# Performance work log

Measured on AMD Instinct MI355X. Metric: run time of the kernel, lower is better.

Reference implementation:

```python
import jax, jax.numpy as jnp
import numpy as np

B, N, D = 4, 4096, 1024

def setup_inputs() -> dict:
    key = jax.random.key(0)
    kx, kql, kqr, kk, kv = jax.random.split(key, 5)
    std = 1.0 / D
    return {
        "x": jax.random.normal(kx, (B, N, D), dtype=jnp.float32),
        "w_query_left": jax.random.normal(kql, (D, D), dtype=jnp.float32) * std,
        "w_query_right": jax.random.normal(kqr, (D, D), dtype=jnp.float32) * std,
        "w_key": jax.random.normal(kk, (D, D), dtype=jnp.float32) * std,
        "w_value": jax.random.normal(kv, (D, D), dtype=jnp.float32) * std,
    }

def reference(x, w_query_left, w_query_right, w_key, w_value):
    # Four dxd projections
    query_left = jnp.einsum('bnd,de->bne', x, w_query_left)
    query_right = jnp.einsum('bnd,de->bne', x, w_query_right)
    key = jnp.einsum('bnd,de->bne', x, w_key)
    value = jnp.einsum('bnd,de->bne', x, w_value)
    # Elementwise gate
    query = query_left * query_right
    # Kernelized attention: key^T @ value, then query @ kv  (dropout p=0 in eval)
    kv_attn = jnp.einsum('bnd,bne->bde', key, value)   # [B, D, D]
    linear_attn = jnp.einsum('bnd,bde->bne', query, kv_attn)
    return linear_attn
```

## Files before the change

kernel.cpp:

```cpp
#include <hip/hip_runtime.h>
#include <stdint.h>

typedef short bf16x8 __attribute__((ext_vector_type(8)));
typedef float f32x4 __attribute__((ext_vector_type(4)));

__device__ __forceinline__ uint16_t f2b(float f) {
    uint32_t u = __builtin_bit_cast(uint32_t, f);
    return (uint16_t)((u + 0x7fffu + ((u >> 16) & 1u)) >> 16);
}

__device__ __forceinline__ void gll16(const void* g, void* l) {
    __builtin_amdgcn_global_load_lds(
        (const __attribute__((address_space(1))) uint32_t*)(uintptr_t)g,
        (__attribute__((address_space(3))) uint32_t*)(uint32_t)(uintptr_t)l,
        16, 0, 0);
}

__global__ __launch_bounds__(256) void cvt_f32_bf16(const float4* __restrict__ in,
                                                    uint2* __restrict__ out, int nvec) {
    int i = blockIdx.x * 256 + threadIdx.x;
    if (i >= nvec) return;
    float4 v = in[i];
    uint2 o;
    o.x = (uint32_t)f2b(v.x) | ((uint32_t)f2b(v.y) << 16);
    o.y = (uint32_t)f2b(v.z) | ((uint32_t)f2b(v.w) << 16);
    out[i] = o;
}

struct Ptr4 { const float* p[4]; };

__global__ __launch_bounds__(256) void tr_w(Ptr4 wp, uint16_t* __restrict__ out) {
    const int m = blockIdx.z;
    const float* in = wp.p[m];
    uint16_t* o = out + (size_t)m * 1048576;
    __shared__ uint16_t tile[64][68];
    int t = threadIdx.x;
    int r0 = blockIdx.y * 64, c0 = blockIdx.x * 64;
    for (int p = 0; p < 4; p++) {
        int row = p * 16 + (t >> 4);
        int c4 = (t & 15) * 4;
        float4 v = *(const float4*)&in[(size_t)(r0 + row) * 1024 + c0 + c4];
        tile[row][c4 + 0] = f2b(v.x);
        tile[row][c4 + 1] = f2b(v.y);
        tile[row][c4 + 2] = f2b(v.z);
        tile[row][c4 + 3] = f2b(v.w);
    }
    __syncthreads();
    for (int p = 0; p < 4; p++) {
        int a = p * 16 + (t >> 4);
        int b4 = (t & 15) * 4;
        uint32_t x0 = tile[b4 + 0][a], x1 = tile[b4 + 1][a];
        uint32_t x2 = tile[b4 + 2][a], x3 = tile[b4 + 3][a];
        uint2 pk;
        pk.x = x0 | (x1 << 16);
        pk.y = x2 | (x3 << 16);
        *(uint2*)&o[(size_t)(c0 + a) * 1024 + r0 + b4] = pk;
    }
}

union SmemP {
    struct { uint16_t lA[4096]; uint16_t lB1[4096]; uint16_t lB2[4096]; } s;
    uint16_t tr[8][32][68];
};

__global__ __launch_bounds__(512, 4) void proj512(const uint16_t* __restrict__ A,
                                                  const uint16_t* __restrict__ Wt,
                                                  uint16_t* __restrict__ Q,
                                                  uint16_t* __restrict__ KT,
                                                  uint16_t* __restrict__ VT) {
    __shared__ SmemP u;
    const int t = threadIdx.x;
    const int wave = t >> 6;
    const int lane = t & 63;
    const int m0 = blockIdx.y * 128;
    const int bx = blockIdx.x;
    const int gate = bx < 8;
    const int e0 = (gate ? bx : bx - 8) * 128;
    const uint16_t* B1 = Wt + (size_t)(gate ? 0 : 2) * 1048576 + (size_t)e0 * 1024;
    const uint16_t* B2 = Wt + (size_t)(gate ? 1 : 3) * 1048576 + (size_t)e0 * 1024;
    const int wm = (wave >> 2) * 64;
    const int we = (wave & 3) * 32;

    const uint16_t* gA = A + (size_t)(m0 + (t >> 2)) * 1024 + (t & 3) * 8;
    const uint16_t* gB1 = B1 + (size_t)(t >> 2) * 1024 + (t & 3) * 8;
    const uint16_t* gB2 = B2 + (size_t)(t >> 2) * 1024 + (t & 3) * 8;
    uint16_t* dA = u.s.lA + wave * 512;
    uint16_t* dB1 = u.s.lB1 + wave * 512;
    uint16_t* dB2 = u.s.lB2 + wave * 512;

    f32x4 acc1[4][2] = {};
    f32x4 acc2[4][2] = {};

    const int arow = wm + (lane & 15);
    const int brow = we + (lane & 15);
    const int koff = (lane >> 4) * 8;

    for (int k0 = 0; k0 < 1024; k0 += 32) {
        __syncthreads();
        gll16(gA + k0, dA);
        gll16(gB1 + k0, dB1);
        gll16(gB2 + k0, dB2);
        __syncthreads();

        bf16x8 af[4], b1f[2], b2f[2];
#pragma unroll
        for (int i = 0; i < 4; i++)
            af[i] = *(const bf16x8*)&u.s.lA[(arow + i * 16) * 32 + koff];
#pragma unroll
        for (int j = 0; j < 2; j++)
            b1f[j] = *(const bf16x8*)&u.s.lB1[(brow + j * 16) * 32 + koff];
#pragma unroll
        for (int j = 0; j < 2; j++)
            b2f[j] = *(const bf16x8*)&u.s.lB2[(brow + j * 16) * 32 + koff];
#pragma unroll
        for (int i = 0; i < 4; i++)
#pragma unroll
            for (int j = 0; j < 2; j++) {
                acc1[i][j] = __builtin_amdgcn_mfma_f32_16x16x32_bf16(af[i], b1f[j],
                                                                     acc1[i][j], 0, 0, 0);
                acc2[i][j] = __builtin_amdgcn_mfma_f32_16x16x32_bf16(af[i], b2f[j],
                                                                     acc2[i][j], 0, 0, 0);
            }
    }

    const int rl = (lane >> 4) * 4;
    const int cl = lane & 15;

    if (gate) {
#pragma unroll
        for (int i = 0; i < 4; i++)
#pragma unroll
            for (int j = 0; j < 2; j++)
#pragma unroll
                for (int r = 0; r < 4; r++) {
                    float g = acc1[i][j][r] * acc2[i][j][r];
                    Q[(size_t)(m0 + wm + i * 16 + rl + r) * 1024 + e0 + we + j * 16 + cl] = f2b(g);
                }
    } else {
        __syncthreads();
        const int batch = m0 >> 12;
        const int tok0 = (m0 & 4095) + wm;
        const int fbase = e0 + we;
        uint16_t* outs[2] = {KT, VT};
        for (int s = 0; s < 2; s++) {
            f32x4(*acc)[2] = (s == 0) ? acc1 : acc2;
#pragma unroll
            for (int i = 0; i < 4; i++)
#pragma unroll
                for (int j = 0; j < 2; j++) {
                    int col = j * 16 + cl;
                    int row0 = i * 16 + rl;
                    uint2 pk;
                    pk.x = (uint32_t)f2b(acc[i][j][0]) | ((uint32_t)f2b(acc[i][j][1]) << 16);
                    pk.y = (uint32_t)f2b(acc[i][j][2]) | ((uint32_t)f2b(acc[i][j][3]) << 16);
                    *(uint2*)&u.tr[wave][col][row0] = pk;
                }
            __builtin_amdgcn_s_waitcnt(0);
            uint16_t* O = outs[s] + (size_t)batch * 4194304;
#pragma unroll
            for (int dd = 0; dd < 8; dd++) {
                int f = dd * 4 + (lane >> 4);
                int t4 = cl * 4;
                uint2 v = *(const uint2*)&u.tr[wave][f][t4];
                *(uint2*)&O[(size_t)(fbase + f) * 4096 + tok0 + t4] = v;
            }
            __builtin_amdgcn_s_waitcnt(0);
        }
    }
}

__global__ __launch_bounds__(256) void gemm_kv_splitk(const uint16_t* __restrict__ VT,
                                                      const uint16_t* __restrict__ KT,
                                                      float* __restrict__ P) {
    const int z = blockIdx.z;
    const int batch = z >> 1, ks = z & 1;
    const uint16_t* Ab = VT + (size_t)batch * 4194304 + ks * 2048;
    const uint16_t* Bb = KT + (size_t)batch * 4194304 + ks * 2048;

    __shared__ uint16_t lA[4096];
    __shared__ uint16_t lB[4096];

    const int t = threadIdx.x;
    const int wave = t >> 6;
    const int lane = t & 63;
    const int m0 = blockIdx.y * 128;
    const int n0 = blockIdx.x * 128;
    const int wm = (wave >> 1) * 64;
    const int wn = (wave & 1) * 64;

    const uint16_t* gA0 = Ab + (size_t)(m0 + (t >> 2)) * 4096 + (t & 3) * 8;
    const uint16_t* gB0 = Bb + (size_t)(n0 + (t >> 2)) * 4096 + (t & 3) * 8;
    uint16_t* lA0 = lA + wave * 512;
    uint16_t* lA1 = lA + 2048 + wave * 512;
    uint16_t* lB0 = lB + wave * 512;
    uint16_t* lB1 = lB + 2048 + wave * 512;

    f32x4 acc[4][4] = {};

    const int arow = wm + (lane & 15);
    const int brow = wn + (lane & 15);
    const int koff = (lane >> 4) * 8;

    for (int k0 = 0; k0 < 2048; k0 += 32) {
        __syncthreads();
        gll16(gA0 + k0, lA0);
        gll16(gA0 + (size_t)64 * 4096 + k0, lA1);
        gll16(gB0 + k0, lB0);
        gll16(gB0 + (size_t)64 * 4096 + k0, lB1);
        __syncthreads();

        bf16x8 af[4], bfr[4];
#pragma unroll
        for (int i = 0; i < 4; i++)
            af[i] = *(const bf16x8*)&lA[(arow + i * 16) * 32 + koff];
#pragma unroll
        for (int i = 0; i < 4; i++)
            bfr[i] = *(const bf16x8*)&lB[(brow + i * 16) * 32 + koff];
#pragma unroll
        for (int i = 0; i < 4; i++)
#pragma unroll
            for (int j = 0; j < 4; j++)
                acc[i][j] = __builtin_amdgcn_mfma_f32_16x16x32_bf16(af[i], bfr[j],
                                                                    acc[i][j], 0, 0, 0);
    }

    float* Pb = P + (size_t)z * 1048576;
    const int crow = m0 + wm + (lane >> 4) * 4;
    const int ccol = n0 + wn + (lane & 15);
#pragma unroll
    for (int i = 0; i < 4; i++)
#pragma unroll
        for (int j = 0; j < 4; j++)
#pragma unroll
            for (int r = 0; r < 4; r++)
                Pb[(size_t)(crow + i * 16 + r) * 1024 + ccol + j * 16] = acc[i][j][r];
}

__global__ __launch_bounds__(256) void reduce_kv(const float4* __restrict__ P,
                                                 uint2* __restrict__ kvT) {
    int i = blockIdx.x * 256 + threadIdx.x;
    int b = i >> 18;
    int r = i & 262143;
    const float4* base = P + (size_t)b * 524288 + r;
    float4 s0 = base[0];
    float4 s1 = base[262144];
    float x = s0.x + s1.x;
    float y = s0.y + s1.y;
    float zz = s0.z + s1.z;
    float w = s0.w + s1.w;
    uint2 o;
    o.x = (uint32_t)f2b(x) | ((uint32_t)f2b(y) << 16);
    o.y = (uint32_t)f2b(zz) | ((uint32_t)f2b(w) << 16);
    kvT[i] = o;
}

__global__ __launch_bounds__(256) void gemm_out(const uint16_t* __restrict__ A,
                                                const uint16_t* __restrict__ Bt,
                                                float* __restrict__ C) {
    const uint16_t* Ab = A + (size_t)blockIdx.z * 4194304;
    const uint16_t* Bb = Bt + (size_t)blockIdx.z * 1048576;

    __shared__ uint16_t lA[4096];
    __shared__ uint16_t lB[4096];

    const int t = threadIdx.x;
    const int wave = t >> 6;
    const int lane = t & 63;
    const int m0 = blockIdx.y * 128;
    const int n0 = blockIdx.x * 128;
    const int wm = (wave >> 1) * 64;
    const int wn = (wave & 1) * 64;

    const uint16_t* gA0 = Ab + (size_t)(m0 + (t >> 2)) * 1024 + (t & 3) * 8;
    const uint16_t* gB0 = Bb + (size_t)(n0 + (t >> 2)) * 1024 + (t & 3) * 8;
    uint16_t* lA0 = lA + wave * 512;
    uint16_t* lA1 = lA + 2048 + wave * 512;
    uint16_t* lB0 = lB + wave * 512;
    uint16_t* lB1 = lB + 2048 + wave * 512;

    f32x4 acc[4][4] = {};

    const int arow = wm + (lane & 15);
    const int brow = wn + (lane & 15);
    const int koff = (lane >> 4) * 8;

    for (int k0 = 0; k0 < 1024; k0 += 32) {
        __syncthreads();
        gll16(gA0 + k0, lA0);
        gll16(gA0 + (size_t)64 * 1024 + k0, lA1);
        gll16(gB0 + k0, lB0);
        gll16(gB0 + (size_t)64 * 1024 + k0, lB1);
        __syncthreads();

        bf16x8 af[4], bfr[4];
#pragma unroll
        for (int i = 0; i < 4; i++)
            af[i] = *(const bf16x8*)&lA[(arow + i * 16) * 32 + koff];
#pragma unroll
        for (int i = 0; i < 4; i++)
            bfr[i] = *(const bf16x8*)&lB[(brow + i * 16) * 32 + koff];
#pragma unroll
        for (int i = 0; i < 4; i++)
#pragma unroll
            for (int j = 0; j < 4; j++)
                acc[i][j] = __builtin_amdgcn_mfma_f32_16x16x32_bf16(af[i], bfr[j],
                                                                    acc[i][j], 0, 0, 0);
    }

    float* Cb = C + (size_t)blockIdx.z * 4194304;
    const int crow = m0 + wm + (lane >> 4) * 4;
    const int ccol = n0 + wn + (lane & 15);
#pragma unroll
    for (int i = 0; i < 4; i++)
#pragma unroll
        for (int j = 0; j < 4; j++)
#pragma unroll
            for (int r = 0; r < 4; r++)
                Cb[(size_t)(crow + i * 16 + r) * 1024 + ccol + j * 16] = acc[i][j][r];
}

extern "C" void kernel_launch(void* const* d_in, const int* in_sizes, int n_in,
                              void* d_out, int out_size, void* d_ws, size_t ws_size,
                              hipStream_t stream) {
    const float* x = (const float*)d_in[0];

    uint16_t* ws = (uint16_t*)d_ws;
    uint16_t* xb  = ws;
    float*    kvP = (float*)d_ws;
    uint16_t* Wt  = ws + 33554432;
    uint16_t* kvT = Wt;
    uint16_t* Q   = ws + 37748736;
    uint16_t* KT  = ws + 54525952;
    uint16_t* VT  = ws + 71303168;

    cvt_f32_bf16<<<16384, 256, 0, stream>>>((const float4*)x, (uint2*)xb, 4194304);

    Ptr4 wp;
    wp.p[0] = (const float*)d_in[1];
    wp.p[1] = (const float*)d_in[2];
    wp.p[2] = (const float*)d_in[3];
    wp.p[3] = (const float*)d_in[4];
    tr_w<<<dim3(16, 16, 4), 256, 0, stream>>>(wp, Wt);

    proj512<<<dim3(16, 128), 512, 0, stream>>>(xb, Wt, Q, KT, VT);

    gemm_kv_splitk<<<dim3(8, 8, 8), 256, 0, stream>>>(VT, KT, kvP);

    reduce_kv<<<4096, 256, 0, stream>>>((const float4*)kvP, (uint2*)kvT);

    gemm_out<<<dim3(8, 32, 4), 256, 0, stream>>>(Q, kvT, (float*)d_out);
}
```

Before: 391.2 us.

## Use 512-thread blocks for kv and output GEMMs, raise kv split-K to four

Both the kv GEMM and the output GEMM now run 8 waves per 128x128 tile, each wave computing a 64x32 sub-tile, so a block issues one global-to-LDS load per operand per thread instead of two. The kv GEMM split-K goes from 2 to 4, doubling its block count to 1024 to fill more compute units, and reduce_kv now sums four partials. The cost is more fp32 partial traffic (16 MB written and read instead of 8 MB) and less register-level reuse per wave, since each wave issues 8 MFMAs per 6 LDS fragment loads instead of 16 per 8.

```diff
diff --git a/kernel.cpp b/kernel.cpp
--- a/kernel.cpp
+++ b/kernel.cpp
@@ -169,13 +169,13 @@
     }
 }
 
-__global__ __launch_bounds__(256) void gemm_kv_splitk(const uint16_t* __restrict__ VT,
-                                                      const uint16_t* __restrict__ KT,
-                                                      float* __restrict__ P) {
+__global__ __launch_bounds__(512, 4) void gemm_kv512(const uint16_t* __restrict__ VT,
+                                                     const uint16_t* __restrict__ KT,
+                                                     float* __restrict__ P) {
     const int z = blockIdx.z;
-    const int batch = z >> 1, ks = z & 1;
-    const uint16_t* Ab = VT + (size_t)batch * 4194304 + ks * 2048;
-    const uint16_t* Bb = KT + (size_t)batch * 4194304 + ks * 2048;
+    const int batch = z >> 2, ks = z & 3;
+    const uint16_t* Ab = VT + (size_t)batch * 4194304 + ks * 1024;
+    const uint16_t* Bb = KT + (size_t)batch * 4194304 + ks * 1024;
 
     __shared__ uint16_t lA[4096];
     __shared__ uint16_t lB[4096];
@@ -185,55 +185,51 @@
     const int lane = t & 63;
     const int m0 = blockIdx.y * 128;
     const int n0 = blockIdx.x * 128;
-    const int wm = (wave >> 1) * 64;
-    const int wn = (wave & 1) * 64;
-
-    const uint16_t* gA0 = Ab + (size_t)(m0 + (t >> 2)) * 4096 + (t & 3) * 8;
-    const uint16_t* gB0 = Bb + (size_t)(n0 + (t >> 2)) * 4096 + (t & 3) * 8;
-    uint16_t* lA0 = lA + wave * 512;
-    uint16_t* lA1 = lA + 2048 + wave * 512;
-    uint16_t* lB0 = lB + wave * 512;
-    uint16_t* lB1 = lB + 2048 + wave * 512;
-
-    f32x4 acc[4][4] = {};
+    const int wm = (wave >> 2) * 64;
+    const int we = (wave & 3) * 32;
+
+    const uint16_t* gA = Ab + (size_t)(m0 + (t >> 2)) * 4096 + (t & 3) * 8;
+    const uint16_t* gB = Bb + (size_t)(n0 + (t >> 2)) * 4096 + (t & 3) * 8;
+    uint16_t* dA = lA + wave * 512;
+    uint16_t* dB = lB + wave * 512;
+
+    f32x4 acc[4][2] = {};
 
     const int arow = wm + (lane & 15);
-    const int brow = wn + (lane & 15);
+    const int brow = we + (lane & 15);
     const int koff = (lane >> 4) * 8;
 
-    for (int k0 = 0; k0 < 2048; k0 += 32) {
-        __syncthreads();
-        gll16(gA0 + k0, lA0);
-        gll16(gA0 + (size_t)64 * 4096 + k0, lA1);
-        gll16(gB0 + k0, lB0);
-        gll16(gB0 + (size_t)64 * 4096 + k0, lB1);
-        __syncthreads();
-
-        bf16x8 af[4], bfr[4];
+    for (int k0 = 0; k0 < 1024; k0 += 32) {
+        __syncthreads();
+        gll16(gA + k0, dA);
+        gll16(gB + k0, dB);
+        __syncthreads();
+
+        bf16x8 af[4], bfr[2];
 #pragma unroll
         for (int i = 0; i < 4; i++)
             af[i] = *(const bf16x8*)&lA[(arow + i * 16) * 32 + koff];
 #pragma unroll
-        for (int i = 0; i < 4; i++)
-            bfr[i] = *(const bf16x8*)&lB[(brow + i * 16) * 32 + koff];
-#pragma unroll
-        for (int i = 0; i < 4; i++)
-#pragma unroll
-            for (int j = 0; j < 4; j++)
+        for (int j = 0; j < 2; j++)
+            bfr[j] = *(const bf16x8*)&lB[(brow + j * 16) * 32 + koff];
+#pragma unroll
+        for (int i = 0; i < 4; i++)
+#pragma unroll
+            for (int j = 0; j < 2; j++)
                 acc[i][j] = __builtin_amdgcn_mfma_f32_16x16x32_bf16(af[i], bfr[j],
                                                                     acc[i][j], 0, 0, 0);
     }
 
     float* Pb = P + (size_t)z * 1048576;
-    const int crow = m0 + wm + (lane >> 4) * 4;
-    const int ccol = n0 + wn + (lane & 15);
+    const int rl = (lane >> 4) * 4;
+    const int cl = lane & 15;
 #pragma unroll
     for (int i = 0; i < 4; i++)
 #pragma unroll
-        for (int j = 0; j < 4; j++)
+        for (int j = 0; j < 2; j++)
 #pragma unroll
             for (int r = 0; r < 4; r++)
-                Pb[(size_t)(crow + i * 16 + r) * 1024 + ccol + j * 16] = acc[i][j][r];
+                Pb[(size_t)(m0 + wm + i * 16 + rl + r) * 1024 + n0 + we + j * 16 + cl] = acc[i][j][r];
 }
 
 __global__ __launch_bounds__(256) void reduce_kv(const float4* __restrict__ P,
@@ -241,22 +237,24 @@
     int i = blockIdx.x * 256 + threadIdx.x;
     int b = i >> 18;
     int r = i & 262143;
-    const float4* base = P + (size_t)b * 524288 + r;
+    const float4* base = P + (size_t)b * 1048576 + r;
     float4 s0 = base[0];
     float4 s1 = base[262144];
-    float x = s0.x + s1.x;
-    float y = s0.y + s1.y;
-    float zz = s0.z + s1.z;
-    float w = s0.w + s1.w;
+    float4 s2 = base[524288];
+    float4 s3 = base[786432];
+    float x = s0.x + s1.x + s2.x + s3.x;
+    float y = s0.y + s1.y + s2.y + s3.y;
+    float zz = s0.z + s1.z + s2.z + s3.z;
+    float w = s0.w + s1.w + s2.w + s3.w;
     uint2 o;
     o.x = (uint32_t)f2b(x) | ((uint32_t)f2b(y) << 16);
     o.y = (uint32_t)f2b(zz) | ((uint32_t)f2b(w) << 16);
     kvT[i] = o;
 }
 
-__global__ __launch_bounds__(256) void gemm_out(const uint16_t* __restrict__ A,
-                                                const uint16_t* __restrict__ Bt,
-                                                float* __restrict__ C) {
+__global__ __launch_bounds__(512, 4) void gemm_out512(const uint16_t* __restrict__ A,
+                                                      const uint16_t* __restrict__ Bt,
+                                                      float* __restrict__ C) {
     const uint16_t* Ab = A + (size_t)blockIdx.z * 4194304;
     const uint16_t* Bb = Bt + (size_t)blockIdx.z * 1048576;
 
@@ -268,55 +266,51 @@
     const int lane = t & 63;
     const int m0 = blockIdx.y * 128;
     const int n0 = blockIdx.x * 128;
-    const int wm = (wave >> 1) * 64;
-    const int wn = (wave & 1) * 64;
-
-    const uint16_t* gA0 = Ab + (size_t)(m0 + (t >> 2)) * 1024 + (t & 3) * 8;
-    const uint16_t* gB0 = Bb + (size_t)(n0 + (t >> 2)) * 1024 + (t & 3) * 8;
-    uint16_t* lA0 = lA + wave * 512;
-    uint16_t* lA1 = lA + 2048 + wave * 512;
-    uint16_t* lB0 = lB + wave * 512;
-    uint16_t* lB1 = lB + 2048 + wave * 512;
-
-    f32x4 acc[4][4] = {};
+    const int wm = (wave >> 2) * 64;
+    const int we = (wave & 3) * 32;
+
+    const uint16_t* gA = Ab + (size_t)(m0 + (t >> 2)) * 1024 + (t & 3) * 8;
+    const uint16_t* gB = Bb + (size_t)(n0 + (t >> 2)) * 1024 + (t & 3) * 8;
+    uint16_t* dA = lA + wave * 512;
+    uint16_t* dB = lB + wave * 512;
+
+    f32x4 acc[4][2] = {};
 
     const int arow = wm + (lane & 15);
-    const int brow = wn + (lane & 15);
+    const int brow = we + (lane & 15);
     const int koff = (lane >> 4) * 8;
 
     for (int k0 = 0; k0 < 1024; k0 += 32) {
         __syncthreads();
-        gll16(gA0 + k0, lA0);
-        gll16(gA0 + (size_t)64 * 1024 + k0, lA1);
-        gll16(gB0 + k0, lB0);
-        gll16(gB0 + (size_t)64 * 1024 + k0, lB1);
-        __syncthreads();
-
-        bf16x8 af[4], bfr[4];
+        gll16(gA + k0, dA);
+        gll16(gB + k0, dB);
+        __syncthreads();
+
+        bf16x8 af[4], bfr[2];
 #pragma unroll
         for (int i = 0; i < 4; i++)
             af[i] = *(const bf16x8*)&lA[(arow + i * 16) * 32 + koff];
 #pragma unroll
-        for (int i = 0; i < 4; i++)
-            bfr[i] = *(const bf16x8*)&lB[(brow + i * 16) * 32 + koff];
-#pragma unroll
-        for (int i = 0; i < 4; i++)
-#pragma unroll
-            for (int j = 0; j < 4; j++)
+        for (int j = 0; j < 2; j++)
+            bfr[j] = *(const bf16x8*)&lB[(brow + j * 16) * 32 + koff];
+#pragma unroll
+        for (int i = 0; i < 4; i++)
+#pragma unroll
+            for (int j = 0; j < 2; j++)
                 acc[i][j] = __builtin_amdgcn_mfma_f32_16x16x32_bf16(af[i], bfr[j],
                                                                     acc[i][j], 0, 0, 0);
     }
 
     float* Cb = C + (size_t)blockIdx.z * 4194304;
-    const int crow = m0 + wm + (lane >> 4) * 4;
-    const int ccol = n0 + wn + (lane & 15);
+    const int rl = (lane >> 4) * 4;
+    const int cl = lane & 15;
 #pragma unroll
     for (int i = 0; i < 4; i++)
 #pragma unroll
-        for (int j = 0; j < 4; j++)
+        for (int j = 0; j < 2; j++)
 #pragma unroll
             for (int r = 0; r < 4; r++)
-                Cb[(size_t)(crow + i * 16 + r) * 1024 + ccol + j * 16] = acc[i][j][r];
+                Cb[(size_t)(m0 + wm + i * 16 + rl + r) * 1024 + n0 + we + j * 16 + cl] = acc[i][j][r];
 }
 
 extern "C" void kernel_launch(void* const* d_in, const int* in_sizes, int n_in,
@@ -344,9 +338,9 @@
 
     proj512<<<dim3(16, 128), 512, 0, stream>>>(xb, Wt, Q, KT, VT);
 
-    gemm_kv_splitk<<<dim3(8, 8, 8), 256, 0, stream>>>(VT, KT, kvP);
+    gemm_kv512<<<dim3(8, 8, 16), 512, 0, stream>>>(VT, KT, kvP);
 
     reduce_kv<<<4096, 256, 0, stream>>>((const float4*)kvP, (uint2*)kvT);
 
-    gemm_out<<<dim3(8, 32, 4), 256, 0, stream>>>(Q, kvT, (float*)d_out);
-}
+    gemm_out512<<<dim3(8, 32, 4), 512, 0, stream>>>(Q, kvT, (float*)d_out);
+}
```

Measured after the change: 405.3 us. 3.6% more time.
